# Optimization experiments

Hardware: AMD Instinct MI355X
Metric: run time of the kernel (lower is better)

Reference implementation:

```python
import jax, jax.numpy as jnp
import numpy as np

MAXHD = 100.0
MAXV = 40.0
LSTM_UNITS = 20
IN_DIM = 12


def setup_inputs() -> dict:
    key = jax.random.key(0)
    ks = jax.random.split(key, 10)
    nveh, nt = 8192, 512
    leadfol_inputs = jax.random.normal(ks[0], (nveh, nt, IN_DIM), dtype=jnp.float32)
    true_traj = jax.random.normal(ks[1], (nveh, nt), dtype=jnp.float32)
    hidden_states = jnp.zeros((2, nveh, LSTM_UNITS), dtype=jnp.float32)
    s = 0.1
    # LSTM kernel/recurrent kernel/bias (keras gate order: i, f, c, o)
    W_k = jax.random.normal(ks[2], (IN_DIM, 4 * LSTM_UNITS), dtype=jnp.float32) * s
    W_r = jax.random.normal(ks[3], (LSTM_UNITS, 4 * LSTM_UNITS), dtype=jnp.float32) * s
    b_l = jnp.zeros((4 * LSTM_UNITS,), dtype=jnp.float32)
    # dense (10, relu) and lc_actions (3)
    W_d = jax.random.normal(ks[4], (LSTM_UNITS, 10), dtype=jnp.float32) * s
    b_d = jnp.zeros((10,), dtype=jnp.float32)
    W_lc = jax.random.normal(ks[5], (10, 3), dtype=jnp.float32) * s
    b_lc = jnp.zeros((3,), dtype=jnp.float32)
    return {"leadfol_inputs": leadfol_inputs, "true_traj": true_traj,
            "hidden_states": hidden_states, "W_k": W_k, "W_r": W_r, "b_l": b_l,
            "W_d": W_d, "b_d": b_d, "W_lc": W_lc, "b_lc": b_lc}


def reference(leadfol_inputs, true_traj, hidden_states, W_k, W_r, b_l, W_d, b_d, W_lc, b_lc):
    # time-major for scan: (nt, nveh, ...)
    lf_t = jnp.swapaxes(leadfol_inputs, 0, 1)
    pos_t = jnp.swapaxes(true_traj, 0, 1)

    def step(carry, xt):
        h, c = carry
        pos, lf = xt  # pos: (nveh,), lf: (nveh, 12)
        lead_hd = (lf[:, :3] - pos[:, None]) / MAXHD
        fol_hd = (pos[:, None] - lf[:, 3:6]) / MAXHD
        spds = lf[:, 6:] / MAXV
        x = jnp.concatenate([lead_hd, fol_hd, spds], axis=1)
        x = jnp.where(jnp.isnan(x), jnp.ones_like(x), x)
        z = x @ W_k + h @ W_r + b_l
        zi, zf, zg, zo = jnp.split(z, 4, axis=1)
        c = jax.nn.sigmoid(zf) * c + jax.nn.sigmoid(zi) * jnp.tanh(zg)
        h = jax.nn.sigmoid(zo) * jnp.tanh(c)
        d = jax.nn.relu(h @ W_d + b_d)
        lc = d @ W_lc + b_lc
        return (h, c), lc

    (h, c), lc_t = jax.lax.scan(step, (hidden_states[0], hidden_states[1]), (pos_t, lf_t))
    pred_lc_action = jnp.swapaxes(lc_t, 0, 1)  # (nveh, nt, 3)
    return (true_traj, pred_lc_action, h, c)
```

## Files before the change

### kernel.cpp

```cpp
#include <hip/hip_runtime.h>

#define NVEH 8192
#define NT   512

typedef short bf16x8 __attribute__((ext_vector_type(8)));
typedef float f32x4  __attribute__((ext_vector_type(4)));

__device__ __forceinline__ float fsig(float x) {
    float e = __builtin_amdgcn_exp2f(-1.44269504f * x);
    return __builtin_amdgcn_rcpf(1.0f + e);
}
__device__ __forceinline__ float ftanh(float x) {
    float e = __builtin_amdgcn_exp2f(-2.88539008f * x);
    return 2.0f * __builtin_amdgcn_rcpf(1.0f + e) - 1.0f;
}
__device__ __forceinline__ unsigned short f2bf(float f) {
    union { float f; unsigned u; } vv; vv.f = f;
    unsigned r = vv.u + 0x7fff + ((vv.u >> 16) & 1);
    return (unsigned short)(r >> 16);
}

__global__ __launch_bounds__(64) void lstm_scan_kernel(
    const float* __restrict__ lead, const float* __restrict__ traj,
    const float* __restrict__ hidden,
    const float* __restrict__ W_k, const float* __restrict__ W_r,
    const float* __restrict__ b_l, const float* __restrict__ W_d,
    const float* __restrict__ b_d, const float* __restrict__ W_lc,
    const float* __restrict__ b_lc,
    float* __restrict__ out_lc, float* __restrict__ out_h, float* __restrict__ out_c)
{
    __shared__ alignas(16) unsigned short hrow[16 * 40];

    const int lane = threadIdx.x;
    const int q    = lane >> 4;
    const int v    = lane & 15;
    const int gv   = blockIdx.x * 16 + v;

    bf16x8 aW[5]; f32x4 cB[5];
    #pragma unroll
    for (int tt = 0; tt < 5; ++tt) {
        #pragma unroll
        for (int j = 0; j < 8; ++j) {
            int k = q * 8 + j;
            int p = 16 * tt + v;
            int u = p >> 2, g = p & 3;
            int col = g * 20 + u;
            float w = (k < 12) ? W_k[k * 80 + col] : W_r[(k - 12) * 80 + col];
            aW[tt][j] = (short)f2bf(w);
        }
        #pragma unroll
        for (int reg = 0; reg < 4; ++reg)
            cB[tt][reg] = b_l[reg * 20 + 4 * tt + q];
    }
    bf16x8 aH; f32x4 cD;
    #pragma unroll
    for (int j = 0; j < 8; ++j) {
        int k = q * 8 + j;
        aH[j] = (v < 10 && k >= 12) ? (short)f2bf(W_d[(k - 12) * 10 + v]) : (short)0;
    }
    #pragma unroll
    for (int reg = 0; reg < 4; ++reg) {
        int m = 4 * q + reg;
        cD[reg] = (m < 10) ? b_d[m] : 0.0f;
    }
    float wlc[4][3]; float pb0[3];
    #pragma unroll
    for (int reg = 0; reg < 4; ++reg) {
        int m = 4 * q + reg;
        #pragma unroll
        for (int j = 0; j < 3; ++j) wlc[reg][j] = (m < 10) ? W_lc[m * 3 + j] : 0.0f;
    }
    #pragma unroll
    for (int j = 0; j < 3; ++j) pb0[j] = (q == 0) ? b_lc[j] : 0.0f;

    float h32[5], cst[5];
    #pragma unroll
    for (int tt = 0; tt < 5; ++tt) {
        int u = 4 * tt + q;
        h32[tt] = hidden[(size_t)gv * 20 + u];
        cst[tt] = hidden[(size_t)NVEH * 20 + (size_t)gv * 20 + u];
    }
    #pragma unroll
    for (int tt = 0; tt < 5; ++tt) {
        int u = 4 * tt + q;
        int idx = (tt == 0) ? u : u + 4;
        hrow[v * 40 + idx] = f2bf(h32[tt]);
    }

    float Ac[4], Bc[4];
    #pragma unroll
    for (int i = 0; i < 4; ++i) {
        int e = 4 * q + i;
        if (e < 3)      { Ac[i] =  0.01f;  Bc[i] = -0.01f; }
        else if (e < 6) { Ac[i] = -0.01f;  Bc[i] =  0.01f; }
        else            { Ac[i] =  0.025f; Bc[i] =  0.0f;  }
    }

    const float* lf = lead + (size_t)gv * NT * 12;
    const float* ps = traj + (size_t)gv * NT;
    float* lcout    = out_lc + (size_t)gv * NT * 3;

    float4 r0 = make_float4(0.f,0.f,0.f,0.f); float p0s = 0.f;
    if (q < 3) r0 = *(const float4*)(lf + q * 4);
    if (q < 2) p0s = ps[0];
    unsigned pk0 = 0, pk1 = 0;
    if (q < 3) {
        float xv[4] = { r0.x, r0.y, r0.z, r0.w };
        #pragma unroll
        for (int i = 0; i < 4; ++i) {
            float x = fmaf(xv[i], Ac[i], p0s * Bc[i]);
            xv[i] = (x == x) ? x : 1.0f;
        }
        pk0 = (unsigned)f2bf(xv[0]) | ((unsigned)f2bf(xv[1]) << 16);
        pk1 = (unsigned)f2bf(xv[2]) | ((unsigned)f2bf(xv[3]) << 16);
    }
    __builtin_amdgcn_wave_barrier();

    bf16x8 bx;
    {
        unsigned s0 = __shfl_down(pk0, 16), s1 = __shfl_down(pk1, 16);
        uint2 hA = make_uint2(0, 0); uint4 hB = make_uint4(0, 0, 0, 0);
        if (q == 1) hA = *(const uint2*)&hrow[v * 40];
        if (q >= 2) hB = *(const uint4*)&hrow[v * 40 + (q == 2 ? 8 : 16)];
        unsigned dw0 = (q == 0) ? pk0 : (q == 1) ? s0   : hB.x;
        unsigned dw1 = (q == 0) ? pk1 : (q == 1) ? s1   : hB.y;
        unsigned dw2 = (q == 0) ? s0  : (q == 1) ? hA.x : hB.z;
        unsigned dw3 = (q == 0) ? s1  : (q == 1) ? hA.y : hB.w;
        uint4 tmp = make_uint4(dw0, dw1, dw2, dw3);
        bx = *(bf16x8*)&tmp;
    }

    float4 rA = make_float4(0.f,0.f,0.f,0.f), rB = make_float4(0.f,0.f,0.f,0.f);
    float pA = 0.f, pB = 0.f;
    if (q < 3) { rA = *(const float4*)(lf + 12 * 1 + q * 4);
                 rB = *(const float4*)(lf + 12 * 2 + q * 4); }
    if (q < 2) { pA = ps[1]; pB = ps[2]; }

    for (int t = 0; t < NT; ++t) {
        f32x4 z[5];
        #pragma unroll
        for (int tt = 0; tt < 5; ++tt)
            z[tt] = __builtin_amdgcn_mfma_f32_16x16x32_bf16(aW[tt], bx, cB[tt], 0, 0, 0);

        #pragma unroll
        for (int tt = 0; tt < 5; ++tt) {
            float si = fsig(z[tt][0]);
            float sf = fsig(z[tt][1]);
            float tg = ftanh(z[tt][2]);
            float so = fsig(z[tt][3]);
            float cn = fmaf(sf, cst[tt], si * tg);
            cst[tt] = cn;
            h32[tt] = so * ftanh(cn);
        }

        #pragma unroll
        for (int tt = 0; tt < 5; ++tt) {
            int u = 4 * tt + q;
            int idx = (tt == 0) ? u : u + 4;
            hrow[v * 40 + idx] = f2bf(h32[tt]);
        }

        if (q < 3) {
            float xv[4] = { rA.x, rA.y, rA.z, rA.w };
            #pragma unroll
            for (int i = 0; i < 4; ++i) {
                float x = fmaf(xv[i], Ac[i], pA * Bc[i]);
                xv[i] = (x == x) ? x : 1.0f;
            }
            pk0 = (unsigned)f2bf(xv[0]) | ((unsigned)f2bf(xv[1]) << 16);
            pk1 = (unsigned)f2bf(xv[2]) | ((unsigned)f2bf(xv[3]) << 16);
        }
        __builtin_amdgcn_wave_barrier();

        bf16x8 bxn;
        {
            unsigned s0 = __shfl_down(pk0, 16), s1 = __shfl_down(pk1, 16);
            uint2 hA = make_uint2(0, 0); uint4 hB = make_uint4(0, 0, 0, 0);
            if (q == 1) hA = *(const uint2*)&hrow[v * 40];
            if (q >= 2) hB = *(const uint4*)&hrow[v * 40 + (q == 2 ? 8 : 16)];
            unsigned dw0 = (q == 0) ? pk0 : (q == 1) ? s0   : hB.x;
            unsigned dw1 = (q == 0) ? pk1 : (q == 1) ? s1   : hB.y;
            unsigned dw2 = (q == 0) ? s0  : (q == 1) ? hA.x : hB.z;
            unsigned dw3 = (q == 0) ? s1  : (q == 1) ? hA.y : hB.w;
            uint4 tmp = make_uint4(dw0, dw1, dw2, dw3);
            bxn = *(bf16x8*)&tmp;
        }

        f32x4 d = __builtin_amdgcn_mfma_f32_16x16x32_bf16(aH, bxn, cD, 0, 0, 0);
        float dr[4];
        #pragma unroll
        for (int reg = 0; reg < 4; ++reg) dr[reg] = fmaxf(d[reg], 0.0f);

        float p[3];
        #pragma unroll
        for (int j = 0; j < 3; ++j) {
            float acc = pb0[j];
            #pragma unroll
            for (int reg = 0; reg < 4; ++reg) acc = fmaf(dr[reg], wlc[reg][j], acc);
            acc += __shfl_xor(acc, 16);
            acc += __shfl_xor(acc, 32);
            p[j] = acc;
        }

        if (q == (t & 3)) {
            float* o = lcout + (size_t)t * 3;
            *(float2*)o = make_float2(p[0], p[1]);
            o[2] = p[2];
        }

        bx = bxn;

        rA = rB; pA = pB;
        int tn = (t + 3 < NT) ? (t + 3) : (NT - 1);
        if (q < 3) rB = *(const float4*)(lf + 12 * tn + q * 4);
        if (q < 2) pB = ps[tn];
        __builtin_amdgcn_wave_barrier();
    }

    #pragma unroll
    for (int tt = 0; tt < 5; ++tt) {
        int u = 4 * tt + q;
        out_h[(size_t)gv * 20 + u] = h32[tt];
        out_c[(size_t)gv * 20 + u] = cst[tt];
    }
}

extern "C" void kernel_launch(void* const* d_in, const int* in_sizes, int n_in,
                              void* d_out, int out_size, void* d_ws, size_t ws_size,
                              hipStream_t stream) {
    const float* lead   = (const float*)d_in[0];
    const float* traj   = (const float*)d_in[1];
    const float* hidden = (const float*)d_in[2];
    const float* W_k    = (const float*)d_in[3];
    const float* W_r    = (const float*)d_in[4];
    const float* b_l    = (const float*)d_in[5];
    const float* W_d    = (const float*)d_in[6];
    const float* b_d    = (const float*)d_in[7];
    const float* W_lc   = (const float*)d_in[8];
    const float* b_lc   = (const float*)d_in[9];

    float* out    = (float*)d_out;
    float* out_tt = out;
    float* out_lc = out + (size_t)NVEH * NT;
    float* out_h  = out_lc + (size_t)NVEH * NT * 3;
    float* out_c  = out_h + (size_t)NVEH * 20;

    hipMemcpyAsync(out_tt, traj, (size_t)NVEH * NT * sizeof(float),
                   hipMemcpyDeviceToDevice, stream);

    lstm_scan_kernel<<<dim3(NVEH / 16), dim3(64), 0, stream>>>(
        lead, traj, hidden, W_k, W_r, b_l, W_d, b_d, W_lc, b_lc,
        out_lc, out_h, out_c);
}
```

Baseline: 796.6 us.

## Split LSTM gate tiles across two waves with double-buffered LDS row

Each 16-vehicle block now uses two wavefronts. The five gate MFMA tiles are split 3/2 between them, input staging stays on wave 0, and the dense/output head moves to wave 1. The combined input-and-hidden row is built in a double-buffered shared array and synchronised with a block barrier each step, replacing the shuffle-based operand assembly. This shortens the serial per-step critical path per wave, at the cost of an s_barrier per timestep and twice as many waves.

```diff
diff --git a/kernel.cpp b/kernel.cpp
--- a/kernel.cpp
+++ b/kernel.cpp
@@ -20,7 +20,13 @@
     return (unsigned short)(r >> 16);
 }
 
-__global__ __launch_bounds__(64) void lstm_scan_kernel(
+__device__ __forceinline__ void lds_barrier() {
+    asm volatile("s_waitcnt lgkmcnt(0)" ::: "memory");
+    __builtin_amdgcn_s_barrier();
+    asm volatile("" ::: "memory");
+}
+
+__global__ __launch_bounds__(128) void lstm_scan_kernel(
     const float* __restrict__ lead, const float* __restrict__ traj,
     const float* __restrict__ hidden,
     const float* __restrict__ W_k, const float* __restrict__ W_r,
@@ -29,62 +35,68 @@
     const float* __restrict__ b_lc,
     float* __restrict__ out_lc, float* __restrict__ out_h, float* __restrict__ out_c)
 {
-    __shared__ alignas(16) unsigned short hrow[16 * 40];
-
-    const int lane = threadIdx.x;
+    __shared__ alignas(16) unsigned short row[2][16][40];
+
+    const int tid  = threadIdx.x;
+    const int wid  = tid >> 6;
+    const int lane = tid & 63;
     const int q    = lane >> 4;
     const int v    = lane & 15;
     const int gv   = blockIdx.x * 16 + v;
 
-    bf16x8 aW[5]; f32x4 cB[5];
-    #pragma unroll
-    for (int tt = 0; tt < 5; ++tt) {
+    const int TTB = wid ? 3 : 0;
+
+    bf16x8 aW[3]; f32x4 cB[3];
+    #pragma unroll
+    for (int l = 0; l < 3; ++l) {
+        if (l < 2 || wid == 0) {
+            const int tt = TTB + l;
+            #pragma unroll
+            for (int j = 0; j < 8; ++j) {
+                int k = q * 8 + j;
+                int p = 16 * tt + v;
+                int u = p >> 2, g = p & 3;
+                int col = g * 20 + u;
+                float w = (k < 12) ? W_k[k * 80 + col] : W_r[(k - 12) * 80 + col];
+                aW[l][j] = (short)f2bf(w);
+            }
+            #pragma unroll
+            for (int reg = 0; reg < 4; ++reg)
+                cB[l][reg] = b_l[reg * 20 + 4 * tt + q];
+        }
+    }
+
+    bf16x8 aH = {};
+    f32x4 cD = {};
+    float wlc[4][3] = {};
+    float pb0[3] = {};
+    if (wid == 1) {
         #pragma unroll
         for (int j = 0; j < 8; ++j) {
             int k = q * 8 + j;
-            int p = 16 * tt + v;
-            int u = p >> 2, g = p & 3;
-            int col = g * 20 + u;
-            float w = (k < 12) ? W_k[k * 80 + col] : W_r[(k - 12) * 80 + col];
-            aW[tt][j] = (short)f2bf(w);
-        }
-        #pragma unroll
-        for (int reg = 0; reg < 4; ++reg)
-            cB[tt][reg] = b_l[reg * 20 + 4 * tt + q];
-    }
-    bf16x8 aH; f32x4 cD;
-    #pragma unroll
-    for (int j = 0; j < 8; ++j) {
-        int k = q * 8 + j;
-        aH[j] = (v < 10 && k >= 12) ? (short)f2bf(W_d[(k - 12) * 10 + v]) : (short)0;
-    }
-    #pragma unroll
-    for (int reg = 0; reg < 4; ++reg) {
-        int m = 4 * q + reg;
-        cD[reg] = (m < 10) ? b_d[m] : 0.0f;
-    }
-    float wlc[4][3]; float pb0[3];
-    #pragma unroll
-    for (int reg = 0; reg < 4; ++reg) {
-        int m = 4 * q + reg;
-        #pragma unroll
-        for (int j = 0; j < 3; ++j) wlc[reg][j] = (m < 10) ? W_lc[m * 3 + j] : 0.0f;
-    }
-    #pragma unroll
-    for (int j = 0; j < 3; ++j) pb0[j] = (q == 0) ? b_lc[j] : 0.0f;
-
-    float h32[5], cst[5];
-    #pragma unroll
-    for (int tt = 0; tt < 5; ++tt) {
-        int u = 4 * tt + q;
-        h32[tt] = hidden[(size_t)gv * 20 + u];
-        cst[tt] = hidden[(size_t)NVEH * 20 + (size_t)gv * 20 + u];
-    }
-    #pragma unroll
-    for (int tt = 0; tt < 5; ++tt) {
-        int u = 4 * tt + q;
-        int idx = (tt == 0) ? u : u + 4;
-        hrow[v * 40 + idx] = f2bf(h32[tt]);
+            aH[j] = (v < 10 && k >= 12) ? (short)f2bf(W_d[(k - 12) * 10 + v]) : (short)0;
+        }
+        #pragma unroll
+        for (int reg = 0; reg < 4; ++reg) {
+            int m = 4 * q + reg;
+            cD[reg] = (m < 10) ? b_d[m] : 0.0f;
+            #pragma unroll
+            for (int j = 0; j < 3; ++j)
+                wlc[reg][j] = (m < 10) ? W_lc[m * 3 + j] : 0.0f;
+        }
+        #pragma unroll
+        for (int j = 0; j < 3; ++j) pb0[j] = (q == 0) ? b_lc[j] : 0.0f;
+    }
+
+    float h32[3], cst[3];
+    #pragma unroll
+    for (int l = 0; l < 3; ++l) {
+        if (l < 2 || wid == 0) {
+            int u = 4 * (TTB + l) + q;
+            h32[l] = hidden[(size_t)gv * 20 + u];
+            cst[l] = hidden[(size_t)NVEH * 20 + (size_t)gv * 20 + u];
+            row[1][v][12 + u] = f2bf(h32[l]);
+        }
     }
 
     float Ac[4], Bc[4];
@@ -100,128 +112,107 @@
     const float* ps = traj + (size_t)gv * NT;
     float* lcout    = out_lc + (size_t)gv * NT * 3;
 
-    float4 r0 = make_float4(0.f,0.f,0.f,0.f); float p0s = 0.f;
-    if (q < 3) r0 = *(const float4*)(lf + q * 4);
-    if (q < 2) p0s = ps[0];
-    unsigned pk0 = 0, pk1 = 0;
-    if (q < 3) {
-        float xv[4] = { r0.x, r0.y, r0.z, r0.w };
-        #pragma unroll
-        for (int i = 0; i < 4; ++i) {
-            float x = fmaf(xv[i], Ac[i], p0s * Bc[i]);
-            xv[i] = (x == x) ? x : 1.0f;
-        }
-        pk0 = (unsigned)f2bf(xv[0]) | ((unsigned)f2bf(xv[1]) << 16);
-        pk1 = (unsigned)f2bf(xv[2]) | ((unsigned)f2bf(xv[3]) << 16);
-    }
-    __builtin_amdgcn_wave_barrier();
-
-    bf16x8 bx;
-    {
-        unsigned s0 = __shfl_down(pk0, 16), s1 = __shfl_down(pk1, 16);
-        uint2 hA = make_uint2(0, 0); uint4 hB = make_uint4(0, 0, 0, 0);
-        if (q == 1) hA = *(const uint2*)&hrow[v * 40];
-        if (q >= 2) hB = *(const uint4*)&hrow[v * 40 + (q == 2 ? 8 : 16)];
-        unsigned dw0 = (q == 0) ? pk0 : (q == 1) ? s0   : hB.x;
-        unsigned dw1 = (q == 0) ? pk1 : (q == 1) ? s1   : hB.y;
-        unsigned dw2 = (q == 0) ? s0  : (q == 1) ? hA.x : hB.z;
-        unsigned dw3 = (q == 0) ? s1  : (q == 1) ? hA.y : hB.w;
-        uint4 tmp = make_uint4(dw0, dw1, dw2, dw3);
-        bx = *(bf16x8*)&tmp;
-    }
-
-    float4 rA = make_float4(0.f,0.f,0.f,0.f), rB = make_float4(0.f,0.f,0.f,0.f);
-    float pA = 0.f, pB = 0.f;
-    if (q < 3) { rA = *(const float4*)(lf + 12 * 1 + q * 4);
-                 rB = *(const float4*)(lf + 12 * 2 + q * 4); }
-    if (q < 2) { pA = ps[1]; pB = ps[2]; }
+    float4 rA = make_float4(0.f,0.f,0.f,0.f), rB = rA, rC = rA;
+    float pA = 0.f, pB = 0.f, pC = 0.f;
+    if (wid == 0) {
+        float4 r0 = make_float4(0.f,0.f,0.f,0.f); float p0s = 0.f;
+        if (q < 3) r0 = *(const float4*)(lf + q * 4);
+        if (q < 2) p0s = ps[0];
+        if (q < 3) {
+            float xv[4] = { r0.x, r0.y, r0.z, r0.w };
+            #pragma unroll
+            for (int i = 0; i < 4; ++i) {
+                float x = fmaf(xv[i], Ac[i], p0s * Bc[i]);
+                xv[i] = (x == x) ? x : 1.0f;
+            }
+            unsigned pk0 = (unsigned)f2bf(xv[0]) | ((unsigned)f2bf(xv[1]) << 16);
+            unsigned pk1 = (unsigned)f2bf(xv[2]) | ((unsigned)f2bf(xv[3]) << 16);
+            *(uint2*)&row[1][v][4 * q] = make_uint2(pk0, pk1);
+        }
+        if (q < 3) {
+            rA = *(const float4*)(lf + 12 * 1 + q * 4);
+            rB = *(const float4*)(lf + 12 * 2 + q * 4);
+            rC = *(const float4*)(lf + 12 * 3 + q * 4);
+        }
+        if (q < 2) { pA = ps[1]; pB = ps[2]; pC = ps[3]; }
+    }
+
+    lds_barrier();
+    bf16x8 bx = *(const bf16x8*)&row[1][v][8 * q];
 
     for (int t = 0; t < NT; ++t) {
-        f32x4 z[5];
-        #pragma unroll
-        for (int tt = 0; tt < 5; ++tt)
-            z[tt] = __builtin_amdgcn_mfma_f32_16x16x32_bf16(aW[tt], bx, cB[tt], 0, 0, 0);
-
-        #pragma unroll
-        for (int tt = 0; tt < 5; ++tt) {
-            float si = fsig(z[tt][0]);
-            float sf = fsig(z[tt][1]);
-            float tg = ftanh(z[tt][2]);
-            float so = fsig(z[tt][3]);
-            float cn = fmaf(sf, cst[tt], si * tg);
-            cst[tt] = cn;
-            h32[tt] = so * ftanh(cn);
-        }
-
-        #pragma unroll
-        for (int tt = 0; tt < 5; ++tt) {
-            int u = 4 * tt + q;
-            int idx = (tt == 0) ? u : u + 4;
-            hrow[v * 40 + idx] = f2bf(h32[tt]);
-        }
-
-        if (q < 3) {
-            float xv[4] = { rA.x, rA.y, rA.z, rA.w };
-            #pragma unroll
-            for (int i = 0; i < 4; ++i) {
-                float x = fmaf(xv[i], Ac[i], pA * Bc[i]);
-                xv[i] = (x == x) ? x : 1.0f;
-            }
-            pk0 = (unsigned)f2bf(xv[0]) | ((unsigned)f2bf(xv[1]) << 16);
-            pk1 = (unsigned)f2bf(xv[2]) | ((unsigned)f2bf(xv[3]) << 16);
-        }
-        __builtin_amdgcn_wave_barrier();
-
-        bf16x8 bxn;
-        {
-            unsigned s0 = __shfl_down(pk0, 16), s1 = __shfl_down(pk1, 16);
-            uint2 hA = make_uint2(0, 0); uint4 hB = make_uint4(0, 0, 0, 0);
-            if (q == 1) hA = *(const uint2*)&hrow[v * 40];
-            if (q >= 2) hB = *(const uint4*)&hrow[v * 40 + (q == 2 ? 8 : 16)];
-            unsigned dw0 = (q == 0) ? pk0 : (q == 1) ? s0   : hB.x;
-            unsigned dw1 = (q == 0) ? pk1 : (q == 1) ? s1   : hB.y;
-            unsigned dw2 = (q == 0) ? s0  : (q == 1) ? hA.x : hB.z;
-            unsigned dw3 = (q == 0) ? s1  : (q == 1) ? hA.y : hB.w;
-            uint4 tmp = make_uint4(dw0, dw1, dw2, dw3);
-            bxn = *(bf16x8*)&tmp;
-        }
-
-        f32x4 d = __builtin_amdgcn_mfma_f32_16x16x32_bf16(aH, bxn, cD, 0, 0, 0);
-        float dr[4];
-        #pragma unroll
-        for (int reg = 0; reg < 4; ++reg) dr[reg] = fmaxf(d[reg], 0.0f);
-
-        float p[3];
-        #pragma unroll
-        for (int j = 0; j < 3; ++j) {
-            float acc = pb0[j];
-            #pragma unroll
-            for (int reg = 0; reg < 4; ++reg) acc = fmaf(dr[reg], wlc[reg][j], acc);
-            acc += __shfl_xor(acc, 16);
-            acc += __shfl_xor(acc, 32);
-            p[j] = acc;
-        }
-
-        if (q == (t & 3)) {
-            float* o = lcout + (size_t)t * 3;
-            *(float2*)o = make_float2(p[0], p[1]);
-            o[2] = p[2];
-        }
-
+        if (wid == 0) {
+            if (q < 3) {
+                float xv[4] = { rA.x, rA.y, rA.z, rA.w };
+                #pragma unroll
+                for (int i = 0; i < 4; ++i) {
+                    float x = fmaf(xv[i], Ac[i], pA * Bc[i]);
+                    xv[i] = (x == x) ? x : 1.0f;
+                }
+                unsigned pk0 = (unsigned)f2bf(xv[0]) | ((unsigned)f2bf(xv[1]) << 16);
+                unsigned pk1 = (unsigned)f2bf(xv[2]) | ((unsigned)f2bf(xv[3]) << 16);
+                *(uint2*)&row[t & 1][v][4 * q] = make_uint2(pk0, pk1);
+            }
+            rA = rB; rB = rC; pA = pB; pB = pC;
+            int tn = (t + 4 < NT) ? (t + 4) : (NT - 1);
+            if (q < 3) rC = *(const float4*)(lf + 12 * tn + q * 4);
+            if (q < 2) pC = ps[tn];
+        }
+
+        f32x4 z[3];
+        z[0] = __builtin_amdgcn_mfma_f32_16x16x32_bf16(aW[0], bx, cB[0], 0, 0, 0);
+        z[1] = __builtin_amdgcn_mfma_f32_16x16x32_bf16(aW[1], bx, cB[1], 0, 0, 0);
+        if (wid == 0)
+            z[2] = __builtin_amdgcn_mfma_f32_16x16x32_bf16(aW[2], bx, cB[2], 0, 0, 0);
+
+        #pragma unroll
+        for (int l = 0; l < 3; ++l) {
+            if (l < 2 || wid == 0) {
+                float si = fsig(z[l][0]);
+                float sf = fsig(z[l][1]);
+                float tg = ftanh(z[l][2]);
+                float so = fsig(z[l][3]);
+                float cn = fmaf(sf, cst[l], si * tg);
+                cst[l] = cn;
+                h32[l] = so * ftanh(cn);
+                row[t & 1][v][12 + 4 * (TTB + l) + q] = f2bf(h32[l]);
+            }
+        }
+
+        lds_barrier();
+        bf16x8 bxn = *(const bf16x8*)&row[t & 1][v][8 * q];
+
+        if (wid == 1) {
+            f32x4 d = __builtin_amdgcn_mfma_f32_16x16x32_bf16(aH, bxn, cD, 0, 0, 0);
+            float dr[4];
+            #pragma unroll
+            for (int reg = 0; reg < 4; ++reg) dr[reg] = fmaxf(d[reg], 0.0f);
+            float p[3];
+            #pragma unroll
+            for (int j = 0; j < 3; ++j) {
+                float acc = pb0[j];
+                #pragma unroll
+                for (int reg = 0; reg < 4; ++reg) acc = fmaf(dr[reg], wlc[reg][j], acc);
+                acc += __shfl_xor(acc, 16);
+                acc += __shfl_xor(acc, 32);
+                p[j] = acc;
+            }
+            if (q == (t & 3)) {
+                float* o = lcout + (size_t)t * 3;
+                *(float2*)o = make_float2(p[0], p[1]);
+                o[2] = p[2];
+            }
+        }
         bx = bxn;
-
-        rA = rB; pA = pB;
-        int tn = (t + 3 < NT) ? (t + 3) : (NT - 1);
-        if (q < 3) rB = *(const float4*)(lf + 12 * tn + q * 4);
-        if (q < 2) pB = ps[tn];
-        __builtin_amdgcn_wave_barrier();
-    }
-
-    #pragma unroll
-    for (int tt = 0; tt < 5; ++tt) {
-        int u = 4 * tt + q;
-        out_h[(size_t)gv * 20 + u] = h32[tt];
-        out_c[(size_t)gv * 20 + u] = cst[tt];
+    }
+
+    #pragma unroll
+    for (int l = 0; l < 3; ++l) {
+        if (l < 2 || wid == 0) {
+            int u = 4 * (TTB + l) + q;
+            out_h[(size_t)gv * 20 + u] = h32[l];
+            out_c[(size_t)gv * 20 + u] = cst[l];
+        }
     }
 }
 
@@ -248,7 +239,7 @@
     hipMemcpyAsync(out_tt, traj, (size_t)NVEH * NT * sizeof(float),
                    hipMemcpyDeviceToDevice, stream);
 
-    lstm_scan_kernel<<<dim3(NVEH / 16), dim3(64), 0, stream>>>(
+    lstm_scan_kernel<<<dim3(NVEH / 16), dim3(128), 0, stream>>>(
         lead, traj, hidden, W_k, W_r, b_l, W_d, b_d, W_lc, b_lc,
         out_lc, out_h, out_c);
 }
```

Result: faster. 722.0 us (-9.4%).
